# Kernel optimization log

Measured on AMD Instinct MI355X. Metric: run time of the kernel, lower is better.

## Reference

```python
import jax, jax.numpy as jnp
import numpy as np

BITS_W = 2  # WAGE default weight bitwidth


def _scale(bits):
    return 2.0 ** (bits - 1)


def quantize_w(x):
    """WAGE Quantize.W: clip to [-1+delta, 1-delta], round to grid of step delta,
    with straight-through estimator for gradients."""
    s = _scale(BITS_W)
    delta = 1.0 / s
    xc = jnp.clip(x, -1.0 + delta, 1.0 - delta)
    y = jnp.round(xc * s) / s
    # straight-through: forward uses y, gradient flows as identity to x
    return x + jax.lax.stop_gradient(y - x)


def setup_inputs() -> dict:
    key = jax.random.key(0)
    k1, k2 = jax.random.split(key)
    B, D_IN, C_OUT = 16384, 1024, 1024
    inputs = jax.random.normal(k1, (B, D_IN), dtype=jnp.float32)
    # learned kernel per build(): shape [d_in, c_out]
    kernel = jax.random.normal(k2, (D_IN, C_OUT), dtype=jnp.float32) * 0.5
    return {"inputs": inputs, "kernel": kernel}


def reference(inputs, kernel):
    # quantize weights every forward pass, then dense matmul
    return jnp.matmul(inputs, quantize_w(kernel))
```

## Files before the change

kernel.cpp:

```cpp
#include <hip/hip_runtime.h>

typedef unsigned short u16;
typedef unsigned int u32;

typedef __bf16 bf16x8 __attribute__((ext_vector_type(8)));
typedef float floatx4 __attribute__((ext_vector_type(4)));


__device__ __forceinline__ u32 f2bf(float f) {
    u32 u = __builtin_bit_cast(u32, f);
    return (u + 0x7fffu + ((u >> 16) & 1u)) >> 16;
}

__device__ __forceinline__ float quant_w(float x) {
    float xc = fminf(fmaxf(x, -0.5f), 0.5f);
    return rintf(xc * 2.0f) * 0.5f;
}

__device__ __forceinline__ void gload_lds16(const u16* g, u16* l) {
    __builtin_amdgcn_global_load_lds(
        (const __attribute__((address_space(1))) void*)g,
        (__attribute__((address_space(3))) void*)l,
        16, 0, 0);
}


__global__ __launch_bounds__(256) void prep_kernel(const float4* __restrict__ Af,
                                                   uint4* __restrict__ Abf,
                                                   const float* __restrict__ W,
                                                   u16* __restrict__ Bt) {
    const int bid = blockIdx.x;
    const int tid = threadIdx.x;
    if (bid < 8192) {
        int t = bid * 256 + tid;
        float4 a = Af[2 * t];
        float4 b = Af[2 * t + 1];
        uint4 o;
        o.x = f2bf(a.x) | (f2bf(a.y) << 16);
        o.y = f2bf(a.z) | (f2bf(a.w) << 16);
        o.z = f2bf(b.x) | (f2bf(b.y) << 16);
        o.w = f2bf(b.z) | (f2bf(b.w) << 16);
        Abf[t] = o;
    } else {
        __shared__ u16 tile[32][33];
        const int KN = 1024;
        int b = bid - 8192;
        int n0 = (b & 31) * 32;
        int k0 = (b >> 5) * 32;
        int tx = tid & 31;
        int ty = tid >> 5;
#pragma unroll
        for (int i = 0; i < 4; i++) {
            int kl = ty + i * 8;
            float x = W[(k0 + kl) * KN + n0 + tx];
            tile[kl][tx] = (u16)f2bf(quant_w(x));
        }
        __syncthreads();
#pragma unroll
        for (int i = 0; i < 4; i++) {
            int nl = ty + i * 8;
            Bt[(n0 + nl) * KN + k0 + tx] = tile[tx][nl];
        }
    }
}


__global__ __launch_bounds__(256) void gemm_bt_kernel(const u16* __restrict__ A,
                                                      const u16* __restrict__ Bt,
                                                      float* __restrict__ C) {
    const int K = 1024;
    const int N = 1024;

    __shared__ alignas(16) u16 As[2][128 * 32];
    __shared__ alignas(16) u16 Bs[2][128 * 32];

    const int tid = threadIdx.x;
    const int mbase = blockIdx.x * 128;
    const int nbase = blockIdx.y * 128;
    const int lane = tid & 63;
    const int wv = tid >> 6;
    const int wm = (wv & 1) * 64;
    const int wn = (wv >> 1) * 64;
    const int frow = lane & 15;
    const int fkc = lane >> 4;
    const int koff = ((fkc ^ ((frow >> 1) & 3)) * 8);

    const int c0 = tid, c1 = tid + 256;
    const int r0 = c0 >> 2, r1 = c1 >> 2;
    const int g0 = (c0 & 3) ^ ((r0 >> 1) & 3);
    const int g1 = (c1 & 3) ^ ((r1 >> 1) & 3);
    const u16* Ag0 = &A[(size_t)(mbase + r0) * K + g0 * 8];
    const u16* Ag1 = &A[(size_t)(mbase + r1) * K + g1 * 8];
    const u16* Bg0 = &Bt[(size_t)(nbase + r0) * K + g0 * 8];
    const u16* Bg1 = &Bt[(size_t)(nbase + r1) * K + g1 * 8];

    floatx4 acc[4][4] = {};

    gload_lds16(Ag0, &As[0][c0 * 8]);
    gload_lds16(Ag1, &As[0][c1 * 8]);
    gload_lds16(Bg0, &Bs[0][c0 * 8]);
    gload_lds16(Bg1, &Bs[0][c1 * 8]);

    for (int it = 0; it < 32; ++it) {
        __syncthreads();
        const int cur = it & 1;
        const int nxt = cur ^ 1;
        if (it + 1 < 32) {
            const int kt = (it + 1) * 32;
            gload_lds16(Ag0 + kt, &As[nxt][c0 * 8]);
            gload_lds16(Ag1 + kt, &As[nxt][c1 * 8]);
            gload_lds16(Bg0 + kt, &Bs[nxt][c0 * 8]);
            gload_lds16(Bg1 + kt, &Bs[nxt][c1 * 8]);
        }

        bf16x8 af[4], bf[4];
#pragma unroll
        for (int i = 0; i < 4; i++)
            af[i] = *(const bf16x8*)&As[cur][(wm + i * 16 + frow) * 32 + koff];
#pragma unroll
        for (int j = 0; j < 4; j++)
            bf[j] = *(const bf16x8*)&Bs[cur][(wn + j * 16 + frow) * 32 + koff];
#pragma unroll
        for (int i = 0; i < 4; i++)
#pragma unroll
            for (int j = 0; j < 4; j++)
                acc[i][j] = __builtin_amdgcn_mfma_f32_16x16x32_bf16(
                    af[i], bf[j], acc[i][j], 0, 0, 0);
    }

    const int crow = (lane >> 4) * 4;
    const int ccol = lane & 15;
#pragma unroll
    for (int i = 0; i < 4; i++) {
#pragma unroll
        for (int j = 0; j < 4; j++) {
            float* cp = &C[(size_t)(mbase + wm + i * 16 + crow) * N + nbase + wn + j * 16 + ccol];
#pragma unroll
            for (int r = 0; r < 4; r++) cp[r * N] = acc[i][j][r];
        }
    }
}


extern "C" void kernel_launch(void* const* d_in, const int* in_sizes, int n_in,
                              void* d_out, int out_size, void* d_ws, size_t ws_size,
                              hipStream_t stream) {
    const float* A = (const float*)d_in[0];
    const float* W = (const float*)d_in[1];
    float* C = (float*)d_out;

    u16* Abf = (u16*)d_ws;
    u16* Btq = (u16*)((char*)d_ws + (size_t)33554432);

    prep_kernel<<<8192 + 1024, 256, 0, stream>>>((const float4*)A, (uint4*)Abf, W, Btq);
    gemm_bt_kernel<<<dim3(128, 8), 256, 0, stream>>>(Abf, Btq, C);
}
```

Measured before the change: 154.9 us.

## Load B fragments directly to registers and deepen A tile to K=64

B operand fragments are now loaded straight from global memory into registers and no longer staged through LDS, while the A tile grows to 64 along K with an 8-way XOR swizzle and double buffering across two named buffers. The main loop is manually unrolled by two so it prefetches the next A stage and the next B registers while computing the current one. This halves the number of barriers per K and removes LDS traffic for B, at the cost of more VGPRs for B fragments and global loads that are not coalesced across lanes.

```diff
diff --git a/kernel.cpp b/kernel.cpp
--- a/kernel.cpp
+++ b/kernel.cpp
@@ -65,14 +65,18 @@
 }
 
 
+struct BF {
+    bf16x8 f[8];
+};
+
 __global__ __launch_bounds__(256) void gemm_bt_kernel(const u16* __restrict__ A,
                                                       const u16* __restrict__ Bt,
                                                       float* __restrict__ C) {
     const int K = 1024;
     const int N = 1024;
 
-    __shared__ alignas(16) u16 As[2][128 * 32];
-    __shared__ alignas(16) u16 Bs[2][128 * 32];
+    __shared__ alignas(16) u16 As0[128 * 64];
+    __shared__ alignas(16) u16 As1[128 * 64];
 
     const int tid = threadIdx.x;
     const int mbase = blockIdx.x * 128;
@@ -83,50 +87,71 @@
     const int wn = (wv >> 1) * 64;
     const int frow = lane & 15;
     const int fkc = lane >> 4;
-    const int koff = ((fkc ^ ((frow >> 1) & 3)) * 8);
+    const int rsw = frow & 7;
 
-    const int c0 = tid, c1 = tid + 256;
-    const int r0 = c0 >> 2, r1 = c1 >> 2;
-    const int g0 = (c0 & 3) ^ ((r0 >> 1) & 3);
-    const int g1 = (c1 & 3) ^ ((r1 >> 1) & 3);
-    const u16* Ag0 = &A[(size_t)(mbase + r0) * K + g0 * 8];
-    const u16* Ag1 = &A[(size_t)(mbase + r1) * K + g1 * 8];
-    const u16* Bg0 = &Bt[(size_t)(nbase + r0) * K + g0 * 8];
-    const u16* Bg1 = &Bt[(size_t)(nbase + r1) * K + g1 * 8];
+    const int srow = tid >> 3;
+    const int g8 = (tid & 7) ^ (srow & 7);
+    const u16* Ag[4];
+#pragma unroll
+    for (int q = 0; q < 4; q++)
+        Ag[q] = &A[(size_t)(mbase + q * 32 + srow) * K + g8 * 8];
+
+    const u16* Bg = &Bt[(size_t)(nbase + wn + frow) * K + fkc * 8];
 
     floatx4 acc[4][4] = {};
 
-    gload_lds16(Ag0, &As[0][c0 * 8]);
-    gload_lds16(Ag1, &As[0][c1 * 8]);
-    gload_lds16(Bg0, &Bs[0][c0 * 8]);
-    gload_lds16(Bg1, &Bs[0][c1 * 8]);
-
-    for (int it = 0; it < 32; ++it) {
-        __syncthreads();
-        const int cur = it & 1;
-        const int nxt = cur ^ 1;
-        if (it + 1 < 32) {
-            const int kt = (it + 1) * 32;
-            gload_lds16(Ag0 + kt, &As[nxt][c0 * 8]);
-            gload_lds16(Ag1 + kt, &As[nxt][c1 * 8]);
-            gload_lds16(Bg0 + kt, &Bs[nxt][c0 * 8]);
-            gload_lds16(Bg1 + kt, &Bs[nxt][c1 * 8]);
-        }
-
-        bf16x8 af[4], bf[4];
+    auto stageA = [&](int kt, u16* __restrict__ dst) {
 #pragma unroll
-        for (int i = 0; i < 4; i++)
-            af[i] = *(const bf16x8*)&As[cur][(wm + i * 16 + frow) * 32 + koff];
+        for (int q = 0; q < 4; q++)
+            gload_lds16(Ag[q] + kt, &dst[(q * 256 + tid) * 8]);
+    };
+    auto loadB = [&](int kt) {
+        BF b;
 #pragma unroll
         for (int j = 0; j < 4; j++)
-            bf[j] = *(const bf16x8*)&Bs[cur][(wn + j * 16 + frow) * 32 + koff];
 #pragma unroll
-        for (int i = 0; i < 4; i++)
+            for (int s = 0; s < 2; s++)
+                b.f[j * 2 + s] = *(const bf16x8*)&Bg[j * 16 * K + kt + s * 32];
+        return b;
+    };
+    auto computeT = [&](const u16* __restrict__ As, const BF& b) {
 #pragma unroll
-            for (int j = 0; j < 4; j++)
-                acc[i][j] = __builtin_amdgcn_mfma_f32_16x16x32_bf16(
-                    af[i], bf[j], acc[i][j], 0, 0, 0);
+        for (int s = 0; s < 2; s++) {
+            bf16x8 af[4];
+#pragma unroll
+            for (int i = 0; i < 4; i++)
+                af[i] = *(const bf16x8*)&As[(wm + i * 16 + frow) * 64 +
+                                            (((s * 4 + fkc) ^ rsw) * 8)];
+#pragma unroll
+            for (int i = 0; i < 4; i++)
+#pragma unroll
+                for (int j = 0; j < 4; j++)
+                    acc[i][j] = __builtin_amdgcn_mfma_f32_16x16x32_bf16(
+                        af[i], b.f[j * 2 + s], acc[i][j], 0, 0, 0);
+        }
+    };
+
+    stageA(0, As0);
+    BF b0 = loadB(0);
+
+#pragma unroll 1
+    for (int d = 0; d < 7; ++d) {
+        const int kt = d * 128;
+        __syncthreads();
+        stageA(kt + 64, As1);
+        BF b1 = loadB(kt + 64);
+        computeT(As0, b0);
+        __syncthreads();
+        stageA(kt + 128, As0);
+        b0 = loadB(kt + 128);
+        computeT(As1, b1);
     }
+    __syncthreads();
+    stageA(960, As1);
+    BF bt = loadB(960);
+    computeT(As0, b0);
+    __syncthreads();
+    computeT(As1, bt);
 
     const int crow = (lane >> 4) * 4;
     const int ccol = lane & 15;
```

Result: slower. 184.3 us (+18.9%).
